# Performance work log

Hardware: AMD Instinct MI355X
Metric: run time of the kernel (lower is better)

Reference implementation:

```python
import jax, jax.numpy as jnp
import numpy as np
from jax import lax

B, C, T, P = 32, 8, 65536, 16  # batch, channels, time, filter order


def setup_inputs() -> dict:
    key = jax.random.key(0)
    kx, ka = jax.random.split(key)
    x = jax.random.normal(kx, (B, C, T), dtype=jnp.float32)
    # denominator coeffs a: shape (B, C, P+1). a[...,0]=1, small tails for stability
    a_tail = 0.03 * jax.random.normal(ka, (B, C, P), dtype=jnp.float32)
    a = jnp.concatenate([jnp.ones((B, C, 1), dtype=jnp.float32), a_tail], axis=-1)
    return {"x": x, "a": a}


def _allpole(x, a):
    # y[t] = x[t] - sum_{k=1..p} a_k * y[t-k], with a normalized by a[...,0]
    a_n = a / a[..., 0:1]
    p = a.shape[-1] - 1
    # buffer holds last p outputs oldest->newest; pair with [a_p, ..., a_1]
    a_rev = jnp.flip(a_n[..., 1:], axis=-1)  # (B, C, p)

    def step(buf, x_t):
        # buf: (B, C, p), x_t: (B, C)
        y_t = x_t - jnp.sum(a_rev * buf, axis=-1)
        buf = jnp.concatenate([buf[..., 1:], y_t[..., None]], axis=-1)
        return buf, y_t

    x_time = jnp.moveaxis(x, -1, 0)  # (T, B, C)
    buf0 = jnp.zeros(x.shape[:-1] + (p,), dtype=x.dtype)
    _, ys = lax.scan(step, buf0, x_time)
    return jnp.moveaxis(ys, 0, -1)  # (B, C, T)


def reference(x, a):
    return _allpole(x, a)
```

## Files before the change

kernel.cpp:

```cpp
#include <hip/hip_runtime.h>


constexpr int B_ = 32;
constexpr int C_ = 8;
constexpr int T_ = 65536;
constexpr int P_ = 16;
constexpr int BC = B_ * C_;
constexpr int L_ = 128;
constexpr int W_ = 320;
constexpr int NCHUNK = T_ / L_;
constexpr int WARM_IT = W_ / 16;
constexpr int OUT_IT = L_ / 16;
constexpr int NTHREADS = BC * NCHUNK;
constexpr int BLOCK = 256;

__global__ __launch_bounds__(BLOCK) void allpole_kernel(
    const float* __restrict__ x, const float* __restrict__ a,
    float* __restrict__ y)
{
    const int gid = blockIdx.x * BLOCK + threadIdx.x;
    const int ch = gid >> 9;
    const int ci = gid & (NCHUNK - 1);

    const float* __restrict__ xc = x + (size_t)ch * T_;
    float* __restrict__ yc = y + (size_t)ch * T_;
    const float* __restrict__ ac = a + ch * (P_ + 1);

    const float inv_a0 = 1.0f / ac[0];
    float b[P_ + 1];
#pragma unroll
    for (int k = 1; k <= P_; ++k) b[k] = -ac[k] * inv_a0;

    float h[16];
#pragma unroll
    for (int i = 0; i < 16; ++i) h[i] = 0.0f;

    const int base = ci * L_ - W_;

#define STEP16(XS, OS, DO_OUT)                                            \
    _Pragma("unroll")                                                     \
    for (int s = 0; s < 16; ++s) {                                        \
        float c0 = fmaf(b[2],  h[(s - 2)  & 15], (XS)[s]);                \
        c0 = fmaf(b[3],  h[(s - 3)  & 15], c0);                           \
        c0 = fmaf(b[4],  h[(s - 4)  & 15], c0);                           \
        c0 = fmaf(b[5],  h[(s - 5)  & 15], c0);                           \
        float c1 = b[6] * h[(s - 6)  & 15];                               \
        c1 = fmaf(b[7],  h[(s - 7)  & 15], c1);                           \
        c1 = fmaf(b[8],  h[(s - 8)  & 15], c1);                           \
        c1 = fmaf(b[9],  h[(s - 9)  & 15], c1);                           \
        float c2 = b[10] * h[(s - 10) & 15];                              \
        c2 = fmaf(b[11], h[(s - 11) & 15], c2);                           \
        c2 = fmaf(b[12], h[(s - 12) & 15], c2);                           \
        c2 = fmaf(b[13], h[(s - 13) & 15], c2);                           \
        float c3 = b[14] * h[(s - 14) & 15];                              \
        c3 = fmaf(b[15], h[(s - 15) & 15], c3);                           \
        c3 = fmaf(b[16], h[(s - 16) & 15], c3);   \
        const float pre = (c0 + c1) + (c2 + c3);                          \
        h[s] = fmaf(b[1], h[(s - 1) & 15], pre);                          \
        if (DO_OUT) (OS)[s] = h[s];                                       \
    }

    for (int it = 0; it < WARM_IT; ++it) {
        const int t0 = base + it * 16;
        float xs[16];
#pragma unroll
        for (int q = 0; q < 4; ++q) {
            const int tq = t0 + q * 4;
            const int tsafe = tq >= 0 ? tq : 0;
            float4 v = *reinterpret_cast<const float4*>(xc + tsafe);
            const bool ok = tq >= 0;
            xs[q * 4 + 0] = ok ? v.x : 0.0f;
            xs[q * 4 + 1] = ok ? v.y : 0.0f;
            xs[q * 4 + 2] = ok ? v.z : 0.0f;
            xs[q * 4 + 3] = ok ? v.w : 0.0f;
        }
        float dummy[16];
        STEP16(xs, dummy, false)
    }

    for (int it = 0; it < OUT_IT; ++it) {
        const int t0 = ci * L_ + it * 16;
        float xs[16];
#pragma unroll
        for (int q = 0; q < 4; ++q) {
            float4 v = *reinterpret_cast<const float4*>(xc + t0 + q * 4);
            xs[q * 4 + 0] = v.x; xs[q * 4 + 1] = v.y;
            xs[q * 4 + 2] = v.z; xs[q * 4 + 3] = v.w;
        }
        float os[16];
        STEP16(xs, os, true)
#pragma unroll
        for (int q = 0; q < 4; ++q) {
            float4 v;
            v.x = os[q * 4 + 0]; v.y = os[q * 4 + 1];
            v.z = os[q * 4 + 2]; v.w = os[q * 4 + 3];
            *reinterpret_cast<float4*>(yc + t0 + q * 4) = v;
        }
    }
#undef STEP16
}

extern "C" void kernel_launch(void* const* d_in, const int* in_sizes, int n_in,
                              void* d_out, int out_size, void* d_ws, size_t ws_size,
                              hipStream_t stream) {
    const float* x = (const float*)d_in[0];
    const float* a = (const float*)d_in[1];
    float* y = (float*)d_out;
    const int grid = NTHREADS / BLOCK;
    allpole_kernel<<<grid, BLOCK, 0, stream>>>(x, a, y);
}
```

Baseline: 165.0 us.

## Halve chunk length, software-prefetch next input block, split warmup clamped path

Halves the output chunk length per thread, which doubles the thread count and parallelism while keeping the same 320-sample warmup, so total recurrence work per output rises. The input loads are software-pipelined: the next 16-sample block is prefetched before computing the current one to hide global memory latency. The warmup loop is split so that only chunks near the start use clamped loads, and launch bounds request higher occupancy. The trade-off is more redundant warmup computation against better latency hiding and occupancy.

```diff
diff --git a/kernel.cpp b/kernel.cpp
--- a/kernel.cpp
+++ b/kernel.cpp
@@ -6,7 +6,7 @@
 constexpr int T_ = 65536;
 constexpr int P_ = 16;
 constexpr int BC = B_ * C_;
-constexpr int L_ = 128;
+constexpr int L_ = 64;
 constexpr int W_ = 320;
 constexpr int NCHUNK = T_ / L_;
 constexpr int WARM_IT = W_ / 16;
@@ -14,12 +14,66 @@
 constexpr int NTHREADS = BC * NCHUNK;
 constexpr int BLOCK = 256;
 
-__global__ __launch_bounds__(BLOCK) void allpole_kernel(
+#define STEP16(XS)                                                        \
+    _Pragma("unroll")                                                     \
+    for (int s = 0; s < 16; ++s) {                                        \
+        float c0 = fmaf(b[2],  h[(s - 2)  & 15], (XS)[s]);                \
+        c0 = fmaf(b[3],  h[(s - 3)  & 15], c0);                           \
+        c0 = fmaf(b[4],  h[(s - 4)  & 15], c0);                           \
+        c0 = fmaf(b[5],  h[(s - 5)  & 15], c0);                           \
+        float c1 = b[6] * h[(s - 6)  & 15];                               \
+        c1 = fmaf(b[7],  h[(s - 7)  & 15], c1);                           \
+        c1 = fmaf(b[8],  h[(s - 8)  & 15], c1);                           \
+        c1 = fmaf(b[9],  h[(s - 9)  & 15], c1);                           \
+        float c2 = b[10] * h[(s - 10) & 15];                              \
+        c2 = fmaf(b[11], h[(s - 11) & 15], c2);                           \
+        c2 = fmaf(b[12], h[(s - 12) & 15], c2);                           \
+        c2 = fmaf(b[13], h[(s - 13) & 15], c2);                           \
+        float c3 = b[14] * h[(s - 14) & 15];                              \
+        c3 = fmaf(b[15], h[(s - 15) & 15], c3);                           \
+        c3 = fmaf(b[16], h[(s - 16) & 15], c3);                           \
+        const float pre = (c0 + c1) + (c2 + c3);                          \
+        h[s] = fmaf(b[1], h[(s - 1) & 15], pre);                          \
+    }
+
+__device__ __forceinline__ void load64B(const float* __restrict__ xc, int t0,
+                                        float4 p[4]) {
+#pragma unroll
+    for (int q = 0; q < 4; ++q)
+        p[q] = *reinterpret_cast<const float4*>(xc + t0 + q * 4);
+}
+
+__device__ __forceinline__ void load64B_clamped(const float* __restrict__ xc,
+                                                int t0, float4 p[4]) {
+#pragma unroll
+    for (int q = 0; q < 4; ++q) {
+        const int tq = t0 + q * 4;
+        const int ts = tq < 0 ? 0 : tq;
+        float4 v = *reinterpret_cast<const float4*>(xc + ts);
+        const bool ok = tq >= 0;
+        p[q].x = ok ? v.x : 0.0f;
+        p[q].y = ok ? v.y : 0.0f;
+        p[q].z = ok ? v.z : 0.0f;
+        p[q].w = ok ? v.w : 0.0f;
+    }
+}
+
+__device__ __forceinline__ void unpack16(const float4 p[4], float xs[16]) {
+#pragma unroll
+    for (int q = 0; q < 4; ++q) {
+        xs[q * 4 + 0] = p[q].x;
+        xs[q * 4 + 1] = p[q].y;
+        xs[q * 4 + 2] = p[q].z;
+        xs[q * 4 + 3] = p[q].w;
+    }
+}
+
+__global__ __launch_bounds__(BLOCK, 4) void allpole_kernel(
     const float* __restrict__ x, const float* __restrict__ a,
     float* __restrict__ y)
 {
     const int gid = blockIdx.x * BLOCK + threadIdx.x;
-    const int ch = gid >> 9;
+    const int ch = gid >> 10;
     const int ci = gid & (NCHUNK - 1);
 
     const float* __restrict__ xc = x + (size_t)ch * T_;
@@ -36,68 +90,43 @@
     for (int i = 0; i < 16; ++i) h[i] = 0.0f;
 
     const int base = ci * L_ - W_;
+    const int obase = ci * L_;
 
-#define STEP16(XS, OS, DO_OUT)                                            \
-    _Pragma("unroll")                                                     \
-    for (int s = 0; s < 16; ++s) {                                        \
-        float c0 = fmaf(b[2],  h[(s - 2)  & 15], (XS)[s]);                \
-        c0 = fmaf(b[3],  h[(s - 3)  & 15], c0);                           \
-        c0 = fmaf(b[4],  h[(s - 4)  & 15], c0);                           \
-        c0 = fmaf(b[5],  h[(s - 5)  & 15], c0);                           \
-        float c1 = b[6] * h[(s - 6)  & 15];                               \
-        c1 = fmaf(b[7],  h[(s - 7)  & 15], c1);                           \
-        c1 = fmaf(b[8],  h[(s - 8)  & 15], c1);                           \
-        c1 = fmaf(b[9],  h[(s - 9)  & 15], c1);                           \
-        float c2 = b[10] * h[(s - 10) & 15];                              \
-        c2 = fmaf(b[11], h[(s - 11) & 15], c2);                           \
-        c2 = fmaf(b[12], h[(s - 12) & 15], c2);                           \
-        c2 = fmaf(b[13], h[(s - 13) & 15], c2);                           \
-        float c3 = b[14] * h[(s - 14) & 15];                              \
-        c3 = fmaf(b[15], h[(s - 15) & 15], c3);                           \
-        c3 = fmaf(b[16], h[(s - 16) & 15], c3);   \
-        const float pre = (c0 + c1) + (c2 + c3);                          \
-        h[s] = fmaf(b[1], h[(s - 1) & 15], pre);                          \
-        if (DO_OUT) (OS)[s] = h[s];                                       \
+    float4 p[4];
+
+    if (base >= 0) {
+        load64B(xc, base, p);
+        for (int it = 0; it < WARM_IT; ++it) {
+            float xs[16];
+            unpack16(p, xs);
+            load64B(xc, base + (it + 1) * 16, p);
+            STEP16(xs)
+        }
+    } else {
+        load64B_clamped(xc, base, p);
+        for (int it = 0; it < WARM_IT; ++it) {
+            float xs[16];
+            unpack16(p, xs);
+            load64B_clamped(xc, base + (it + 1) * 16, p);
+            STEP16(xs)
+        }
     }
 
-    for (int it = 0; it < WARM_IT; ++it) {
-        const int t0 = base + it * 16;
+    for (int ot = 0; ot < OUT_IT; ++ot) {
         float xs[16];
-#pragma unroll
-        for (int q = 0; q < 4; ++q) {
-            const int tq = t0 + q * 4;
-            const int tsafe = tq >= 0 ? tq : 0;
-            float4 v = *reinterpret_cast<const float4*>(xc + tsafe);
-            const bool ok = tq >= 0;
-            xs[q * 4 + 0] = ok ? v.x : 0.0f;
-            xs[q * 4 + 1] = ok ? v.y : 0.0f;
-            xs[q * 4 + 2] = ok ? v.z : 0.0f;
-            xs[q * 4 + 3] = ok ? v.w : 0.0f;
-        }
-        float dummy[16];
-        STEP16(xs, dummy, false)
-    }
-
-    for (int it = 0; it < OUT_IT; ++it) {
-        const int t0 = ci * L_ + it * 16;
-        float xs[16];
-#pragma unroll
-        for (int q = 0; q < 4; ++q) {
-            float4 v = *reinterpret_cast<const float4*>(xc + t0 + q * 4);
-            xs[q * 4 + 0] = v.x; xs[q * 4 + 1] = v.y;
-            xs[q * 4 + 2] = v.z; xs[q * 4 + 3] = v.w;
-        }
-        float os[16];
-        STEP16(xs, os, true)
+        unpack16(p, xs);
+        const int tn = (ot < OUT_IT - 1) ? obase + (ot + 1) * 16 : obase;
+        load64B(xc, tn, p);
+        STEP16(xs)
+        const int t0 = obase + ot * 16;
 #pragma unroll
         for (int q = 0; q < 4; ++q) {
             float4 v;
-            v.x = os[q * 4 + 0]; v.y = os[q * 4 + 1];
-            v.z = os[q * 4 + 2]; v.w = os[q * 4 + 3];
+            v.x = h[q * 4 + 0]; v.y = h[q * 4 + 1];
+            v.z = h[q * 4 + 2]; v.w = h[q * 4 + 3];
             *reinterpret_cast<float4*>(yc + t0 + q * 4) = v;
         }
     }
-#undef STEP16
 }
 
 extern "C" void kernel_launch(void* const* d_in, const int* in_sizes, int n_in,
```

After: 205.9 us. +24.8%, slower.
